# Kernel optimization log

Hardware: AMD Instinct MI355X
Metric: run time of the kernel (lower is better)

The kernel has to match this reference:

```python
import jax, jax.numpy as jnp
import numpy as np

N = 100000       # nodes
E = 3200000      # directed edges (avg_degree ~32)
F_IN = 512
H = 16
C = 7


def setup_inputs() -> dict:
    key = jax.random.key(0)
    k1, k2, k3, k4 = jax.random.split(key, 4)
    x = jax.random.normal(k1, (N, F_IN), dtype=jnp.float32)
    edge_index = jax.random.randint(k2, (2, E), 0, N, dtype=jnp.int32)
    # Glorot-ish init for weights
    W1 = jax.random.normal(k3, (F_IN, H), dtype=jnp.float32) * (1.0 / np.sqrt(F_IN))
    b1 = jnp.zeros((H,), dtype=jnp.float32)
    W2 = jax.random.normal(k4, (H, C), dtype=jnp.float32) * (1.0 / np.sqrt(H))
    b2 = jnp.zeros((C,), dtype=jnp.float32)
    return {"x": x, "edge_index": edge_index, "W1": W1, "b1": b1, "W2": W2, "b2": b2}


def _gcn_prep(edge_index, n):
    # add self-loops (PyG GCNConv default: add_self_loops=True)
    loop = jnp.arange(n, dtype=edge_index.dtype)
    src = jnp.concatenate([edge_index[0], loop])  # [E+N]
    dst = jnp.concatenate([edge_index[1], loop])  # [E+N]
    # symmetric normalization deg^{-1/2} (A+I) deg^{-1/2}; deg over targets
    deg = jax.ops.segment_sum(jnp.ones_like(dst, dtype=jnp.float32), dst, num_segments=n)
    dinv = jax.lax.rsqrt(jnp.maximum(deg, 1.0))  # deg >= 1 due to self-loops
    norm = dinv[src] * dinv[dst]                 # [E+N]
    return src, dst, norm


def _gcn_conv(h, src, dst, norm, W, b, n):
    h = h @ W                                            # [N, out] transform first (small out dim)
    msg = h[src] * norm[:, None]                         # gather + scale, [E+N, out]
    out = jax.ops.segment_sum(msg, dst, num_segments=n)  # scatter-add
    return out + b


def reference(x, edge_index, W1, b1, W2, b2):
    n = x.shape[0]
    src, dst, norm = _gcn_prep(edge_index, n)
    h = _gcn_conv(x, src, dst, norm, W1, b1, n)
    h = jax.nn.relu(h)
    # F.dropout(training=self.training) is identity in eval mode
    h = _gcn_conv(h, src, dst, norm, W2, b2, n)
    return jax.nn.log_softmax(h, axis=1)
```

## Files before the change

kernel.cpp:

```cpp
#include <hip/hip_runtime.h>
#include <math.h>

#define F_IN 512
#define H1 16
#define C_OUT 7
#define BSHIFT 7
#define BNODES 128
#define SRCMASK 0x1FFFFu
#define P3CAP 5120

__global__ __launch_bounds__(1024) void k_fill_p1(const int* __restrict__ dst,
                                                  int* __restrict__ cnt, int E, int B) {
    __shared__ int lh[1024];
    int t = threadIdx.x;
    for (int i = t; i < B; i += 1024) lh[i] = 0;
    __syncthreads();
    int e0 = blockIdx.x * 4096;
#pragma unroll
    for (int k = 0; k < 4; k++) {
        int e = e0 + t + 1024 * k;
        if (e < E) atomicAdd(&lh[dst[e] >> BSHIFT], 1);
    }
    __syncthreads();
    for (int i = t; i < B; i += 1024) cnt[(size_t)blockIdx.x * B + i] = lh[i];
}

__global__ __launch_bounds__(256) void k_colscan(const int* __restrict__ cnt,
                                                 int* __restrict__ base,
                                                 int* __restrict__ btotal, int nfb, int B) {
    int b = blockIdx.x;
    int t = threadIdx.x;
    int loc[4];
    int s = 0;
    int j0 = t * 4;
#pragma unroll
    for (int k = 0; k < 4; k++) {
        int j = j0 + k;
        int v = (j < nfb) ? cnt[(size_t)j * B + b] : 0;
        loc[k] = s;
        s += v;
    }
    __shared__ int sh[256];
    sh[t] = s;
    __syncthreads();
    for (int off = 1; off < 256; off <<= 1) {
        int v2 = (t >= off) ? sh[t - off] : 0;
        __syncthreads();
        sh[t] += v2;
        __syncthreads();
    }
    int excl = sh[t] - s;
#pragma unroll
    for (int k = 0; k < 4; k++) {
        int j = j0 + k;
        if (j < nfb) base[(size_t)j * B + b] = excl + loc[k];
    }
    if (t == 255) btotal[b] = sh[255];
}

__global__ __launch_bounds__(1024) void k_sscan(const int* __restrict__ btotal,
                                                int* __restrict__ bstart, int B, int E) {
    __shared__ int s[1024];
    int t = threadIdx.x;
    int v = (t < B) ? btotal[t] : 0;
    s[t] = v;
    __syncthreads();
    for (int off = 1; off < 1024; off <<= 1) {
        int x = (t >= off) ? s[t - off] : 0;
        __syncthreads();
        s[t] += x;
        __syncthreads();
    }
    if (t < B) bstart[t] = s[t] - v;
    if (t == 0) bstart[B] = E;
}

__global__ __launch_bounds__(1024) void k_fill_p2(
    const int* __restrict__ src, const int* __restrict__ dst,
    const int* __restrict__ base, const int* __restrict__ bstart,
    unsigned* __restrict__ bedge, int E, int B) {
    __shared__ int lh[1024];
    __shared__ int scan[1024];
    __shared__ int gb[1024];
    __shared__ unsigned lsort[4096];
    __shared__ unsigned short lbk[4096];
    int t = threadIdx.x;
    for (int i = t; i < B; i += 1024) lh[i] = 0;
    __syncthreads();
    int e0 = blockIdx.x * 4096;
    int myb[4], myr[4];
    unsigned myv[4];
#pragma unroll
    for (int k = 0; k < 4; k++) {
        int e = e0 + t + 1024 * k;
        myb[k] = -1;
        if (e < E) {
            int d = dst[e];
            int b = d >> BSHIFT;
            myb[k] = b;
            myv[k] = ((unsigned)(d & (BNODES - 1)) << 17) | (unsigned)src[e];
            myr[k] = atomicAdd(&lh[b], 1);
        }
    }
    __syncthreads();
    int v = (t < B) ? lh[t] : 0;
    scan[t] = v;
    __syncthreads();
    for (int off = 1; off < 1024; off <<= 1) {
        int x = (t >= off) ? scan[t - off] : 0;
        __syncthreads();
        scan[t] += x;
        __syncthreads();
    }
    scan[t] -= v;
    __syncthreads();
    if (t < B) gb[t] = bstart[t] + base[(size_t)blockIdx.x * B + t];
    __syncthreads();
#pragma unroll
    for (int k = 0; k < 4; k++) {
        if (myb[k] >= 0) {
            int slot = scan[myb[k]] + myr[k];
            lsort[slot] = myv[k];
            lbk[slot] = (unsigned short)myb[k];
        }
    }
    __syncthreads();
    int elim = min(4096, E - e0);
    for (int i = t; i < elim; i += 1024) {
        int b = lbk[i];
        bedge[gb[b] + (i - scan[b])] = lsort[i];
    }
}

__global__ __launch_bounds__(256) void k_fill_p3(
    const int* __restrict__ bstart, const unsigned* __restrict__ bedge,
    int* __restrict__ csr_src, int* __restrict__ indeg, int* __restrict__ rowptr,
    float* __restrict__ dinv, int n) {
    __shared__ int lh[BNODES];
    __shared__ int off[BNODES];
    __shared__ int lc[BNODES];
    __shared__ int sc[BNODES];
    __shared__ int lsort[P3CAP];
    int t = threadIdx.x;
    int bb = blockIdx.x;
    int nodebase = bb << BSHIFT;
    int gs = bstart[bb];
    int ge = bstart[bb + 1];
    for (int i = t; i < BNODES; i += 256) { lh[i] = 0; lc[i] = 0; }
    __syncthreads();
    for (int e = gs + t; e < ge; e += 256) {
        unsigned v = bedge[e];
        atomicAdd(&lh[v >> 17], 1);
    }
    __syncthreads();
    int sv = (t < BNODES) ? lh[t] : 0;
    if (t < BNODES) sc[t] = sv;
    __syncthreads();
    for (int o = 1; o < BNODES; o <<= 1) {
        int x = (t < BNODES && t >= o) ? sc[t - o] : 0;
        __syncthreads();
        if (t < BNODES) sc[t] += x;
        __syncthreads();
    }
    if (t < BNODES) off[t] = sc[t] - sv;
    __syncthreads();
    if (t < BNODES) {
        int node = nodebase + t;
        if (node < n) {
            indeg[node] = sv;
            rowptr[node] = gs + off[t];
            dinv[node] = rsqrtf(1.0f + (float)sv);
        }
    }
    for (int e = gs + t; e < ge; e += 256) {
        unsigned v = bedge[e];
        int dl = (int)(v >> 17);
        int rank = atomicAdd(&lc[dl], 1);
        int pos = off[dl] + rank;
        int svv = (int)(v & SRCMASK);
        if (pos < P3CAP) lsort[pos] = svv;
        else csr_src[gs + pos] = svv;
    }
    __syncthreads();
    int lim = min(ge - gs, P3CAP);
    for (int i = t; i < lim; i += 256) csr_src[gs + i] = lsort[i];
}

template<int KH>
__device__ __forceinline__ void gemm1_half(const float* __restrict__ xs,
                                           const float* __restrict__ W1,
                                           int kc, int lrow, float* __restrict__ acc) {
#pragma unroll 4
    for (int k = 0; k < 32; k++) {
        float xv = xs[(KH + k) * 129 + lrow];
        const float* w = W1 + (kc + KH + k) * H1;
#pragma unroll
        for (int c = 0; c < H1; c++) acc[c] = fmaf(xv, w[c], acc[c]);
    }
}

__global__ __launch_bounds__(256) void k_gemm1(
    const float* __restrict__ x, const float* __restrict__ W1,
    const float* __restrict__ dinv, float* __restrict__ g1, int n) {
    __shared__ float xs[64 * 129];
    const int t = threadIdx.x;
    const int rowbase = blockIdx.x * 128;
    const int lrow = t & 127;
    const int kh = t >> 7;

    float acc[H1];
#pragma unroll
    for (int c = 0; c < H1; c++) acc[c] = 0.0f;

    for (int kc = 0; kc < F_IN; kc += 64) {
        __syncthreads();
#pragma unroll
        for (int jj = 0; jj < 8; jj++) {
            int f = t + 256 * jj;
            int r = f >> 4;
            int kq = f & 15;
            int grow = rowbase + r;
            float4 v = *(const float4*)(x + (size_t)min(grow, n - 1) * F_IN + kc + kq * 4);
            xs[(kq * 4 + 0) * 129 + r] = v.x;
            xs[(kq * 4 + 1) * 129 + r] = v.y;
            xs[(kq * 4 + 2) * 129 + r] = v.z;
            xs[(kq * 4 + 3) * 129 + r] = v.w;
        }
        __syncthreads();
        if (kh == 0) gemm1_half<0>(xs, W1, kc, lrow, acc);
        else         gemm1_half<32>(xs, W1, kc, lrow, acc);
    }
    __syncthreads();
    float* red = xs;
    if (kh == 1) {
#pragma unroll
        for (int c = 0; c < H1; c++) red[lrow * H1 + c] = acc[c];
    }
    __syncthreads();
    if (kh == 0) {
        int grow = rowbase + lrow;
        if (grow < n) {
            float d = dinv[grow];
#pragma unroll
            for (int c4 = 0; c4 < 4; c4++) {
                float4 o;
                o.x = (acc[c4 * 4 + 0] + red[lrow * H1 + c4 * 4 + 0]) * d;
                o.y = (acc[c4 * 4 + 1] + red[lrow * H1 + c4 * 4 + 1]) * d;
                o.z = (acc[c4 * 4 + 2] + red[lrow * H1 + c4 * 4 + 2]) * d;
                o.w = (acc[c4 * 4 + 3] + red[lrow * H1 + c4 * 4 + 3]) * d;
                *(float4*)(g1 + (size_t)grow * H1 + c4 * 4) = o;
            }
        }
    }
}

__global__ __launch_bounds__(256) void k_agg1(
    const int* __restrict__ rowptr, const int* __restrict__ indeg,
    const int* __restrict__ csr_src, const float* __restrict__ g1,
    const float* __restrict__ dinv, const float* __restrict__ b1,
    float* __restrict__ r1, int n) {
    int t = threadIdx.x;
    int node = blockIdx.x * 16 + (t >> 4);
    int c = t & 15;
    if (node >= n) return;
    int start = rowptr[node];
    int end = start + indeg[node];
    float s0 = g1[(size_t)node * H1 + c];
    float s1 = 0.f, s2 = 0.f, s3 = 0.f, s4 = 0.f, s5 = 0.f, s6 = 0.f, s7 = 0.f;
    int i = start;
    for (; i + 8 <= end; i += 8) {
        int a0 = csr_src[i + 0], a1 = csr_src[i + 1], a2 = csr_src[i + 2], a3 = csr_src[i + 3];
        int a4 = csr_src[i + 4], a5 = csr_src[i + 5], a6 = csr_src[i + 6], a7 = csr_src[i + 7];
        s0 += g1[(size_t)a0 * H1 + c];
        s1 += g1[(size_t)a1 * H1 + c];
        s2 += g1[(size_t)a2 * H1 + c];
        s3 += g1[(size_t)a3 * H1 + c];
        s4 += g1[(size_t)a4 * H1 + c];
        s5 += g1[(size_t)a5 * H1 + c];
        s6 += g1[(size_t)a6 * H1 + c];
        s7 += g1[(size_t)a7 * H1 + c];
    }
    for (; i < end; i++) s0 += g1[(size_t)csr_src[i] * H1 + c];
    float sum = ((s0 + s1) + (s2 + s3)) + ((s4 + s5) + (s6 + s7));
    float val = fmaf(dinv[node], sum, b1[c]);
    r1[(size_t)node * H1 + c] = fmaxf(val, 0.f);
}

__global__ __launch_bounds__(256) void k_gemm2(
    const float* __restrict__ r1, const float* __restrict__ W2,
    const float* __restrict__ dinv, float* __restrict__ g2, int n) {
    __shared__ float xs[16 * 257];
    const int tid = threadIdx.x;
    const int rowbase = blockIdx.x * 256;
    const int row = rowbase + tid;

#pragma unroll
    for (int j = 0; j < 4; j++) {
        int flat = tid + 256 * j;
        int r = flat >> 2;
        int kq = flat & 3;
        int grow = rowbase + r;
        float4 v = make_float4(0.f, 0.f, 0.f, 0.f);
        if (grow < n) v = *(const float4*)(r1 + (size_t)grow * H1 + kq * 4);
        xs[(kq * 4 + 0) * 257 + r] = v.x;
        xs[(kq * 4 + 1) * 257 + r] = v.y;
        xs[(kq * 4 + 2) * 257 + r] = v.z;
        xs[(kq * 4 + 3) * 257 + r] = v.w;
    }
    __syncthreads();

    float acc[C_OUT];
#pragma unroll
    for (int c = 0; c < C_OUT; c++) acc[c] = 0.0f;
#pragma unroll
    for (int k = 0; k < H1; k++) {
        float xv = xs[k * 257 + tid];
        const float* w = W2 + k * C_OUT;
#pragma unroll
        for (int c = 0; c < C_OUT; c++) acc[c] = fmaf(xv, w[c], acc[c]);
    }

    if (row < n) {
        float d = dinv[row];
#pragma unroll
        for (int c = 0; c < C_OUT; c++) g2[(size_t)row * 8 + c] = acc[c] * d;
        g2[(size_t)row * 8 + 7] = 0.0f;
    }
}

__global__ __launch_bounds__(256) void k_agg2(
    const int* __restrict__ rowptr, const int* __restrict__ indeg,
    const int* __restrict__ csr_src, const float* __restrict__ g2,
    const float* __restrict__ dinv, const float* __restrict__ b2,
    float* __restrict__ out, int n) {
    int t = threadIdx.x;
    int node = blockIdx.x * 32 + (t >> 3);
    int c = t & 7;
    if (node >= n) return;
    int start = rowptr[node];
    int end = start + indeg[node];
    float s0 = (c < C_OUT) ? g2[(size_t)node * 8 + c] : 0.f;
    float s1 = 0.f, s2 = 0.f, s3 = 0.f, s4 = 0.f, s5 = 0.f, s6 = 0.f, s7 = 0.f;
    int i = start;
    for (; i + 8 <= end; i += 8) {
        int a0 = csr_src[i + 0], a1 = csr_src[i + 1], a2 = csr_src[i + 2], a3 = csr_src[i + 3];
        int a4 = csr_src[i + 4], a5 = csr_src[i + 5], a6 = csr_src[i + 6], a7 = csr_src[i + 7];
        s0 += g2[(size_t)a0 * 8 + c];
        s1 += g2[(size_t)a1 * 8 + c];
        s2 += g2[(size_t)a2 * 8 + c];
        s3 += g2[(size_t)a3 * 8 + c];
        s4 += g2[(size_t)a4 * 8 + c];
        s5 += g2[(size_t)a5 * 8 + c];
        s6 += g2[(size_t)a6 * 8 + c];
        s7 += g2[(size_t)a7 * 8 + c];
    }
    for (; i < end; i++) s0 += g2[(size_t)csr_src[i] * 8 + c];
    float sum = ((s0 + s1) + (s2 + s3)) + ((s4 + s5) + (s6 + s7));
    float bc = (c < C_OUT) ? b2[c] : 0.f;
    float val = fmaf(dinv[node], sum, bc);

    float vv = (c < C_OUT) ? val : -1e30f;
    float m = vv;
#pragma unroll
    for (int o = 1; o < 8; o <<= 1) m = fmaxf(m, __shfl_xor(m, o, 8));
    float ex = (c < C_OUT) ? expf(val - m) : 0.f;
    float se = ex;
#pragma unroll
    for (int o = 1; o < 8; o <<= 1) se += __shfl_xor(se, o, 8);
    float l = logf(se) + m;
    if (c < C_OUT) out[(size_t)node * C_OUT + c] = val - l;
}

extern "C" void kernel_launch(void* const* d_in, const int* in_sizes, int n_in,
                              void* d_out, int out_size, void* d_ws, size_t ws_size,
                              hipStream_t stream) {
    const float* x  = (const float*)d_in[0];
    const int* ei   = (const int*)d_in[1];
    const float* W1 = (const float*)d_in[2];
    const float* b1 = (const float*)d_in[3];
    const float* W2 = (const float*)d_in[4];
    const float* b2 = (const float*)d_in[5];
    float* out = (float*)d_out;

    const int n = in_sizes[0] / F_IN;
    const int E = in_sizes[1] / 2;
    const int* src = ei;
    const int* dst = ei + E;

    const int B   = (n + BNODES - 1) >> BSHIFT;
    const int nfb = (E + 4095) >> 12;

    int*   indeg    = (int*)d_ws;
    int*   rowptr   = indeg + n;
    float* dinv     = (float*)(rowptr + n);
    int*   btotal   = (int*)(dinv + n);
    int*   bstart   = btotal + B;
    int*   cnt      = bstart + B + 1;
    int*   base     = cnt + (size_t)nfb * B;
    float* g1       = (float*)(base + (size_t)nfb * B);
    float* r1       = g1 + (size_t)16 * n;
    unsigned* bedge = (unsigned*)(r1 + (size_t)16 * n);
    int*   csr_src  = (int*)(bedge + E);
    float* g2 = g1;

    const int nbN = (n + 255) / 256;

    k_fill_p1<<<nfb, 1024, 0, stream>>>(dst, cnt, E, B);
    k_colscan<<<B, 256, 0, stream>>>(cnt, base, btotal, nfb, B);
    k_sscan<<<1, 1024, 0, stream>>>(btotal, bstart, B, E);
    k_fill_p2<<<nfb, 1024, 0, stream>>>(src, dst, base, bstart, bedge, E, B);
    k_fill_p3<<<B, 256, 0, stream>>>(bstart, bedge, csr_src, indeg, rowptr, dinv, n);

    k_gemm1<<<(n + 127) / 128, 256, 0, stream>>>(x, W1, dinv, g1, n);
    k_agg1<<<(n + 15) / 16, 256, 0, stream>>>(rowptr, indeg, csr_src, g1, dinv, b1, r1, n);
    k_gemm2<<<nbN, 256, 0, stream>>>(r1, W2, dinv, g2, n);
    k_agg2<<<(n + 31) / 32, 256, 0, stream>>>(rowptr, indeg, csr_src, g2, dinv, b2, out, n);
}
```

Measured before the change: 453.3 us.

## Fuse layer-2 GEMM into agg1 and vectorize gathers with edge-parallel lanes

Folds the second dense transform (r1 @ W2, dinv scaling) into the first aggregation kernel, removing the r1 round-trip through memory and one kernel launch. Both aggregation kernels now gather float4 rows with several lanes splitting a node's edges, combining partial sums with shuffles. agg2 also stages log-softmax results in shared memory so the output store is coalesced. The cost is extra shuffle reductions and more registers for the W2 values held per thread.

```diff
diff --git a/kernel.cpp b/kernel.cpp
--- a/kernel.cpp
+++ b/kernel.cpp
@@ -258,73 +258,78 @@
     const int* __restrict__ rowptr, const int* __restrict__ indeg,
     const int* __restrict__ csr_src, const float* __restrict__ g1,
     const float* __restrict__ dinv, const float* __restrict__ b1,
-    float* __restrict__ r1, int n) {
+    const float* __restrict__ W2, float* __restrict__ g2, int n) {
     int t = threadIdx.x;
     int node = blockIdx.x * 16 + (t >> 4);
-    int c = t & 15;
+    int l = t & 15;
+    int eo = l >> 2;
+    int c4 = l & 3;
     if (node >= n) return;
+
+    float w[4][C_OUT];
+#pragma unroll
+    for (int kk = 0; kk < 4; kk++)
+#pragma unroll
+        for (int c = 0; c < C_OUT; c++)
+            w[kk][c] = W2[(c4 * 4 + kk) * C_OUT + c];
+    float4 b1c = *(const float4*)(b1 + c4 * 4);
+
     int start = rowptr[node];
     int end = start + indeg[node];
-    float s0 = g1[(size_t)node * H1 + c];
-    float s1 = 0.f, s2 = 0.f, s3 = 0.f, s4 = 0.f, s5 = 0.f, s6 = 0.f, s7 = 0.f;
-    int i = start;
-    for (; i + 8 <= end; i += 8) {
-        int a0 = csr_src[i + 0], a1 = csr_src[i + 1], a2 = csr_src[i + 2], a3 = csr_src[i + 3];
-        int a4 = csr_src[i + 4], a5 = csr_src[i + 5], a6 = csr_src[i + 6], a7 = csr_src[i + 7];
-        s0 += g1[(size_t)a0 * H1 + c];
-        s1 += g1[(size_t)a1 * H1 + c];
-        s2 += g1[(size_t)a2 * H1 + c];
-        s3 += g1[(size_t)a3 * H1 + c];
-        s4 += g1[(size_t)a4 * H1 + c];
-        s5 += g1[(size_t)a5 * H1 + c];
-        s6 += g1[(size_t)a6 * H1 + c];
-        s7 += g1[(size_t)a7 * H1 + c];
-    }
-    for (; i < end; i++) s0 += g1[(size_t)csr_src[i] * H1 + c];
-    float sum = ((s0 + s1) + (s2 + s3)) + ((s4 + s5) + (s6 + s7));
-    float val = fmaf(dinv[node], sum, b1[c]);
-    r1[(size_t)node * H1 + c] = fmaxf(val, 0.f);
-}
-
-__global__ __launch_bounds__(256) void k_gemm2(
-    const float* __restrict__ r1, const float* __restrict__ W2,
-    const float* __restrict__ dinv, float* __restrict__ g2, int n) {
-    __shared__ float xs[16 * 257];
-    const int tid = threadIdx.x;
-    const int rowbase = blockIdx.x * 256;
-    const int row = rowbase + tid;
-
-#pragma unroll
-    for (int j = 0; j < 4; j++) {
-        int flat = tid + 256 * j;
-        int r = flat >> 2;
-        int kq = flat & 3;
-        int grow = rowbase + r;
-        float4 v = make_float4(0.f, 0.f, 0.f, 0.f);
-        if (grow < n) v = *(const float4*)(r1 + (size_t)grow * H1 + kq * 4);
-        xs[(kq * 4 + 0) * 257 + r] = v.x;
-        xs[(kq * 4 + 1) * 257 + r] = v.y;
-        xs[(kq * 4 + 2) * 257 + r] = v.z;
-        xs[(kq * 4 + 3) * 257 + r] = v.w;
-    }
-    __syncthreads();
-
-    float acc[C_OUT];
-#pragma unroll
-    for (int c = 0; c < C_OUT; c++) acc[c] = 0.0f;
-#pragma unroll
-    for (int k = 0; k < H1; k++) {
-        float xv = xs[k * 257 + tid];
-        const float* w = W2 + k * C_OUT;
-#pragma unroll
-        for (int c = 0; c < C_OUT; c++) acc[c] = fmaf(xv, w[c], acc[c]);
-    }
-
-    if (row < n) {
-        float d = dinv[row];
-#pragma unroll
-        for (int c = 0; c < C_OUT; c++) g2[(size_t)row * 8 + c] = acc[c] * d;
-        g2[(size_t)row * 8 + 7] = 0.0f;
+    float d = dinv[node];
+
+    float4 s = make_float4(0.f, 0.f, 0.f, 0.f);
+    if (eo == 0) s = *(const float4*)(g1 + (size_t)node * H1 + c4 * 4);
+
+    int i = start + eo;
+    for (; i + 4 < end; i += 8) {
+        int a0 = csr_src[i];
+        int a1 = csr_src[i + 4];
+        float4 v0 = *(const float4*)(g1 + (size_t)a0 * H1 + c4 * 4);
+        float4 v1 = *(const float4*)(g1 + (size_t)a1 * H1 + c4 * 4);
+        s.x += v0.x + v1.x;
+        s.y += v0.y + v1.y;
+        s.z += v0.z + v1.z;
+        s.w += v0.w + v1.w;
+    }
+    if (i < end) {
+        int a = csr_src[i];
+        float4 v = *(const float4*)(g1 + (size_t)a * H1 + c4 * 4);
+        s.x += v.x; s.y += v.y; s.z += v.z; s.w += v.w;
+    }
+
+    s.x += __shfl_xor(s.x, 4); s.y += __shfl_xor(s.y, 4);
+    s.z += __shfl_xor(s.z, 4); s.w += __shfl_xor(s.w, 4);
+    s.x += __shfl_xor(s.x, 8); s.y += __shfl_xor(s.y, 8);
+    s.z += __shfl_xor(s.z, 8); s.w += __shfl_xor(s.w, 8);
+
+    float4 r;
+    r.x = fmaxf(fmaf(d, s.x, b1c.x), 0.f);
+    r.y = fmaxf(fmaf(d, s.y, b1c.y), 0.f);
+    r.z = fmaxf(fmaf(d, s.z, b1c.z), 0.f);
+    r.w = fmaxf(fmaf(d, s.w, b1c.w), 0.f);
+
+    float p[C_OUT];
+#pragma unroll
+    for (int c = 0; c < C_OUT; c++) {
+        p[c] = r.x * w[0][c];
+        p[c] = fmaf(r.y, w[1][c], p[c]);
+        p[c] = fmaf(r.z, w[2][c], p[c]);
+        p[c] = fmaf(r.w, w[3][c], p[c]);
+    }
+#pragma unroll
+    for (int c = 0; c < C_OUT; c++) {
+        p[c] += __shfl_xor(p[c], 1);
+        p[c] += __shfl_xor(p[c], 2);
+    }
+
+    if (eo == 0 && c4 == 0) {
+        float4 o = make_float4(d * p[0], d * p[1], d * p[2], d * p[3]);
+        *(float4*)(g2 + (size_t)node * 8) = o;
+    }
+    if (eo == 0 && c4 == 1) {
+        float4 o = make_float4(d * p[4], d * p[5], d * p[6], 0.0f);
+        *(float4*)(g2 + (size_t)node * 8 + 4) = o;
     }
 }
 
@@ -333,42 +338,77 @@
     const int* __restrict__ csr_src, const float* __restrict__ g2,
     const float* __restrict__ dinv, const float* __restrict__ b2,
     float* __restrict__ out, int n) {
-    int t = threadIdx.x;
-    int node = blockIdx.x * 32 + (t >> 3);
-    int c = t & 7;
-    if (node >= n) return;
-    int start = rowptr[node];
-    int end = start + indeg[node];
-    float s0 = (c < C_OUT) ? g2[(size_t)node * 8 + c] : 0.f;
-    float s1 = 0.f, s2 = 0.f, s3 = 0.f, s4 = 0.f, s5 = 0.f, s6 = 0.f, s7 = 0.f;
-    int i = start;
-    for (; i + 8 <= end; i += 8) {
-        int a0 = csr_src[i + 0], a1 = csr_src[i + 1], a2 = csr_src[i + 2], a3 = csr_src[i + 3];
-        int a4 = csr_src[i + 4], a5 = csr_src[i + 5], a6 = csr_src[i + 6], a7 = csr_src[i + 7];
-        s0 += g2[(size_t)a0 * 8 + c];
-        s1 += g2[(size_t)a1 * 8 + c];
-        s2 += g2[(size_t)a2 * 8 + c];
-        s3 += g2[(size_t)a3 * 8 + c];
-        s4 += g2[(size_t)a4 * 8 + c];
-        s5 += g2[(size_t)a5 * 8 + c];
-        s6 += g2[(size_t)a6 * 8 + c];
-        s7 += g2[(size_t)a7 * 8 + c];
-    }
-    for (; i < end; i++) s0 += g2[(size_t)csr_src[i] * 8 + c];
-    float sum = ((s0 + s1) + (s2 + s3)) + ((s4 + s5) + (s6 + s7));
-    float bc = (c < C_OUT) ? b2[c] : 0.f;
-    float val = fmaf(dinv[node], sum, bc);
-
-    float vv = (c < C_OUT) ? val : -1e30f;
-    float m = vv;
-#pragma unroll
-    for (int o = 1; o < 8; o <<= 1) m = fmaxf(m, __shfl_xor(m, o, 8));
-    float ex = (c < C_OUT) ? expf(val - m) : 0.f;
-    float se = ex;
-#pragma unroll
-    for (int o = 1; o < 8; o <<= 1) se += __shfl_xor(se, o, 8);
-    float l = logf(se) + m;
-    if (c < C_OUT) out[(size_t)node * C_OUT + c] = val - l;
+    __shared__ float ls[32 * C_OUT];
+    int t = threadIdx.x;
+    int g = t >> 3;
+    int node = blockIdx.x * 32 + g;
+    int l = t & 7;
+    int eo = l >> 1;
+    int ch = l & 1;
+
+    float4 s = make_float4(0.f, 0.f, 0.f, 0.f);
+    float d = 0.f;
+    bool valid = node < n;
+    if (valid) {
+        int start = rowptr[node];
+        int end = start + indeg[node];
+        d = dinv[node];
+        if (eo == 0) s = *(const float4*)(g2 + (size_t)node * 8 + ch * 4);
+        int i = start + eo;
+        for (; i + 4 < end; i += 8) {
+            int a0 = csr_src[i];
+            int a1 = csr_src[i + 4];
+            float4 v0 = *(const float4*)(g2 + (size_t)a0 * 8 + ch * 4);
+            float4 v1 = *(const float4*)(g2 + (size_t)a1 * 8 + ch * 4);
+            s.x += v0.x + v1.x;
+            s.y += v0.y + v1.y;
+            s.z += v0.z + v1.z;
+            s.w += v0.w + v1.w;
+        }
+        if (i < end) {
+            int a = csr_src[i];
+            float4 v = *(const float4*)(g2 + (size_t)a * 8 + ch * 4);
+            s.x += v.x; s.y += v.y; s.z += v.z; s.w += v.w;
+        }
+    }
+    s.x += __shfl_xor(s.x, 2); s.y += __shfl_xor(s.y, 2);
+    s.z += __shfl_xor(s.z, 2); s.w += __shfl_xor(s.w, 2);
+    s.x += __shfl_xor(s.x, 4); s.y += __shfl_xor(s.y, 4);
+    s.z += __shfl_xor(s.z, 4); s.w += __shfl_xor(s.w, 4);
+
+    float4 val;
+    if (ch == 0) {
+        float4 bb = *(const float4*)b2;
+        val.x = fmaf(d, s.x, bb.x);
+        val.y = fmaf(d, s.y, bb.y);
+        val.z = fmaf(d, s.z, bb.z);
+        val.w = fmaf(d, s.w, bb.w);
+    } else {
+        val.x = fmaf(d, s.x, b2[4]);
+        val.y = fmaf(d, s.y, b2[5]);
+        val.z = fmaf(d, s.z, b2[6]);
+        val.w = 0.f;
+    }
+    float m = fmaxf(fmaxf(val.x, val.y), val.z);
+    if (ch == 0) m = fmaxf(m, val.w);
+    m = fmaxf(m, __shfl_xor(m, 1));
+    float e0 = expf(val.x - m), e1 = expf(val.y - m), e2 = expf(val.z - m);
+    float e3 = (ch == 0) ? expf(val.w - m) : 0.f;
+    float se = (e0 + e1) + (e2 + e3);
+    se += __shfl_xor(se, 1);
+    float lg = logf(se) + m;
+
+    if (valid && eo == 0) {
+        float* o = ls + g * C_OUT + ch * 4;
+        o[0] = val.x - lg;
+        o[1] = val.y - lg;
+        o[2] = val.z - lg;
+        if (ch == 0) o[3] = val.w - lg;
+    }
+    __syncthreads();
+    int nbase = blockIdx.x * 32;
+    int nv = (n - nbase < 32 ? n - nbase : 32) * C_OUT;
+    if (t < nv) out[(size_t)nbase * C_OUT + t] = ls[t];
 }
 
 extern "C" void kernel_launch(void* const* d_in, const int* in_sizes, int n_in,
@@ -398,12 +438,9 @@
     int*   cnt      = bstart + B + 1;
     int*   base     = cnt + (size_t)nfb * B;
     float* g1       = (float*)(base + (size_t)nfb * B);
-    float* r1       = g1 + (size_t)16 * n;
-    unsigned* bedge = (unsigned*)(r1 + (size_t)16 * n);
+    float* g2       = g1 + (size_t)16 * n;
+    unsigned* bedge = (unsigned*)(g2 + (size_t)16 * n);
     int*   csr_src  = (int*)(bedge + E);
-    float* g2 = g1;
-
-    const int nbN = (n + 255) / 256;
 
     k_fill_p1<<<nfb, 1024, 0, stream>>>(dst, cnt, E, B);
     k_colscan<<<B, 256, 0, stream>>>(cnt, base, btotal, nfb, B);
@@ -412,7 +449,6 @@
     k_fill_p3<<<B, 256, 0, stream>>>(bstart, bedge, csr_src, indeg, rowptr, dinv, n);
 
     k_gemm1<<<(n + 127) / 128, 256, 0, stream>>>(x, W1, dinv, g1, n);
-    k_agg1<<<(n + 15) / 16, 256, 0, stream>>>(rowptr, indeg, csr_src, g1, dinv, b1, r1, n);
-    k_gemm2<<<nbN, 256, 0, stream>>>(r1, W2, dinv, g2, n);
+    k_agg1<<<(n + 15) / 16, 256, 0, stream>>>(rowptr, indeg, csr_src, g1, dinv, b1, W2, g2, n);
     k_agg2<<<(n + 31) / 32, 256, 0, stream>>>(rowptr, indeg, csr_src, g2, dinv, b2, out, n);
 }
```

Measured after the change: 441.6 us. 1.03x faster.
